# Kernel optimization log

Measured on AMD Instinct MI355X. Metric: run time of the kernel, lower is better.

## Reference

```python
import jax, jax.numpy as jnp
import numpy as np
import math

B, S, D = 16, 2048, 128

def setup_inputs() -> dict:
    key = jax.random.key(0)
    k1, k2, k3, k4 = jax.random.split(key, 4)
    query = jax.random.normal(k1, (B, S, D), dtype=jnp.float32)
    key_t = jax.random.normal(k2, (B, S, D), dtype=jnp.float32)
    value = jax.random.normal(k3, (B, S, D), dtype=jnp.float32)
    attn_mask = jax.random.randint(k4, (B, S, S), 0, 2).astype(bool)
    return {"query": query, "key": key_t, "value": value, "attn_mask": attn_mask}

def reference(query, key, value, attn_mask):
    # score = Q K^T / sqrt(d)  -> [B, Sq, Sk]
    scale = 1.0 / math.sqrt(query.shape[-1])
    score = jnp.einsum('bqd,bkd->bqk', query, key) * scale
    # faithful quirk: masked positions are replaced by the VALUE 1e-9 (not -inf)
    mask_score = jnp.where(attn_mask, jnp.float32(1e-9), score)
    # faithful quirk: softmax over dim=1 (the query axis), as in the torch source
    score_matrix = jax.nn.softmax(mask_score, axis=1)
    # output = softmax(scores) @ V  -> [B, Sq, D]
    output = jnp.einsum('bqk,bkd->bqd', score_matrix, value)
    return output
```

## Files before the change

### kernel.cpp

```cpp
#include <hip/hip_runtime.h>
#include <math.h>

#define NB 16
#define SS 2048
#define DQ 128
#define SCALE 0.08838834764831845f

typedef __bf16 bf16x8 __attribute__((ext_vector_type(8)));
typedef unsigned short ushort8_t __attribute__((ext_vector_type(8)));
typedef float floatx4 __attribute__((ext_vector_type(4)));

__device__ __forceinline__ unsigned short f2bf(float x) {
  unsigned int u = __float_as_uint(x);
  u += 0x7fffu + ((u >> 16) & 1u);
  return (unsigned short)(u >> 16);
}
union FragU { ushort8_t u; bf16x8 b; };
__device__ __forceinline__ bf16x8 ld_frag(const unsigned short* p) {
  FragU t; t.u = *(const ushort8_t*)p; return t.b;
}
__device__ __forceinline__ floatx4 mfma16(bf16x8 a, bf16x8 b, floatx4 c) {
  return __builtin_amdgcn_mfma_f32_16x16x32_bf16(a, b, c, 0, 0, 0);
}

__device__ __forceinline__ void bar_lds() {
  asm volatile("s_waitcnt lgkmcnt(0)\n\ts_barrier" ::: "memory");
}


__global__ void zero_accum(float* __restrict__ O) {
  float* p = O + (size_t)blockIdx.x * SS * DQ + 16 * DQ;
#pragma unroll
  for (int i = 0; i < 8; ++i) p[threadIdx.x + 256 * i] = 0.f;
}

__global__ __launch_bounds__(256, 4) void pass1_colsum(
    const float* __restrict__ Q, const float* __restrict__ K,
    const int* __restrict__ M, float* __restrict__ O)
{
  const int k0  = blockIdx.x * 64;
  const int b   = blockIdx.y;
  const int qc  = blockIdx.z;
  const int tid = threadIdx.x;
  const int w = tid >> 6, lane = tid & 63, l15 = lane & 15, quad = lane >> 4;

  __shared__ unsigned short Kbf[64][136];
  __shared__ unsigned short Qbf[64][136];
  __shared__ float red[4][64];

  const float* Qb = Q + (size_t)b * SS * DQ;
  const float* Kb = K + (size_t)b * SS * DQ;
  const int*   Mb = M + (size_t)b * SS * SS;

  const int srow = tid >> 5;
  const int sc4  = (tid & 31) * 4;

#pragma unroll
  for (int r = 0; r < 8; ++r) {
    int row = srow + r * 8;
    float4 v = *(const float4*)(Kb + (size_t)(k0 + row) * DQ + sc4);
    *(ushort4*)&Kbf[row][sc4] = make_ushort4(f2bf(v.x), f2bf(v.y), f2bf(v.z), f2bf(v.w));
  }

  const int qlane = 16 * w + l15;

  float4 qreg[8];
  int4 mv_nxt[4];
  {
    const int q0 = qc * 512;
#pragma unroll
    for (int r = 0; r < 8; ++r)
      qreg[r] = *(const float4*)(Qb + (size_t)(q0 + srow + r * 8) * DQ + sc4);
#pragma unroll
    for (int i = 0; i < 4; ++i)
      mv_nxt[i] = *(const int4*)(Mb + (size_t)(q0 + qlane) * SS + k0 + 16 * i + quad * 4);
  }

  float colacc[16];
#pragma unroll
  for (int t = 0; t < 16; ++t) colacc[t] = 0.f;

  for (int qi = 0; qi < 8; ++qi) {
    bar_lds();
    int4 mv[4] = {mv_nxt[0], mv_nxt[1], mv_nxt[2], mv_nxt[3]};
#pragma unroll
    for (int r = 0; r < 8; ++r) {
      float4 v = qreg[r];
      *(ushort4*)&Qbf[srow + r * 8][sc4] =
          make_ushort4(f2bf(v.x), f2bf(v.y), f2bf(v.z), f2bf(v.w));
    }
    bar_lds();
    if (qi < 7) {
      const int qn = qc * 512 + (qi + 1) * 64;
#pragma unroll
      for (int r = 0; r < 8; ++r)
        qreg[r] = *(const float4*)(Qb + (size_t)(qn + srow + r * 8) * DQ + sc4);
#pragma unroll
      for (int i = 0; i < 4; ++i)
        mv_nxt[i] = *(const int4*)(Mb + (size_t)(qn + qlane) * SS + k0 + 16 * i + quad * 4);
    }

    floatx4 acc[4];
#pragma unroll
    for (int i = 0; i < 4; ++i) acc[i] = (floatx4){0.f, 0.f, 0.f, 0.f};
#pragma unroll
    for (int d0 = 0; d0 < DQ; d0 += 32) {
      bf16x8 bq = ld_frag(&Qbf[qlane][d0 + quad * 8]);
#pragma unroll
      for (int i = 0; i < 4; ++i) {
        bf16x8 ak = ld_frag(&Kbf[16 * i + l15][d0 + quad * 8]);
        acc[i] = mfma16(ak, bq, acc[i]);
      }
    }
#pragma unroll
    for (int i = 0; i < 4; ++i) {
      int mm[4] = {mv[i].x, mv[i].y, mv[i].z, mv[i].w};
#pragma unroll
      for (int r = 0; r < 4; ++r) {
        float s = mm[r] ? 1e-9f : acc[i][r] * SCALE;
        colacc[i * 4 + r] += __expf(s);
      }
    }
  }

#pragma unroll
  for (int t = 0; t < 16; ++t) {
    colacc[t] += __shfl_xor(colacc[t], 1, 64);
    colacc[t] += __shfl_xor(colacc[t], 2, 64);
    colacc[t] += __shfl_xor(colacc[t], 4, 64);
    colacc[t] += __shfl_xor(colacc[t], 8, 64);
  }
  if (l15 == 0) {
#pragma unroll
    for (int i = 0; i < 4; ++i)
#pragma unroll
      for (int r = 0; r < 4; ++r)
        red[w][16 * i + quad * 4 + r] = colacc[i * 4 + r];
  }
  bar_lds();
  if (tid < 64) {
    float s = red[0][tid] + red[1][tid] + red[2][tid] + red[3][tid];
    atomicAdd(O + (size_t)b * SS * DQ + 16 * DQ + k0 + tid, s);
  }
}

__global__ void combine_linv(float* __restrict__ O) {
  const int b  = blockIdx.x;
  const int jb = blockIdx.y * 4;
  float* Ob = O + (size_t)b * SS * DQ;
#pragma unroll
  for (int it = 0; it < 8; ++it) {
    int k = threadIdx.x + 256 * it;
    float inv = 1.0f / Ob[16 * DQ + k];
#pragma unroll
    for (int j = 0; j < 4; ++j)
      Ob[(size_t)(64 * (jb + j)) * DQ + k] = inv;
  }
}

__global__ __launch_bounds__(256, 2) void pass2_out(
    const float* __restrict__ Q, const float* __restrict__ K,
    const float* __restrict__ V, const int* __restrict__ M,
    float* __restrict__ O)
{
  const int b = blockIdx.y, q0 = blockIdx.x * 64;
  const int tid = threadIdx.x;
  const int w = tid >> 6, lane = tid & 63, l15 = lane & 15, quad = lane >> 4;

  __shared__ unsigned short Kbf[64][136];
  __shared__ unsigned short Es[64][72];
  __shared__ unsigned short Wt[128][72];
  __shared__ float Li[SS];

  const float* Qb = Q + (size_t)b * SS * DQ;
  const float* Kb = K + (size_t)b * SS * DQ;
  const float* Vb = V + (size_t)b * SS * DQ;
  const int*   Mb = M + (size_t)b * SS * SS;

  const int srow = tid >> 5;
  const int sc4  = (tid & 31) * 4;

  {
    const float* src = O + ((size_t)b * SS + q0) * DQ;
#pragma unroll
    for (int r = 0; r < 2; ++r) {
      int idx = (tid + r * 256) * 4;
      *(float4*)&Li[idx] = *(const float4*)(src + idx);
    }
  }
  FragU qf[4];
  {
    const float* qrow = Qb + (size_t)(q0 + 16 * w + l15) * DQ;
#pragma unroll
    for (int i = 0; i < 4; ++i) {
      float4 a = *(const float4*)(qrow + 32 * i + quad * 8);
      float4 c = *(const float4*)(qrow + 32 * i + quad * 8 + 4);
      qf[i].u = (ushort8_t){f2bf(a.x), f2bf(a.y), f2bf(a.z), f2bf(a.w),
                            f2bf(c.x), f2bf(c.y), f2bf(c.z), f2bf(c.w)};
    }
  }

  floatx4 accO[8];
#pragma unroll
  for (int j = 0; j < 8; ++j) accO[j] = (floatx4){0.f, 0.f, 0.f, 0.f};

  const int* mrow = Mb + (size_t)(q0 + 16 * w + l15) * SS;

  float4 kreg[8], vreg[8];
  int4 mv_nxt[4];
  const int vk2 = (tid >> 5) * 2;
  {
#pragma unroll
    for (int r = 0; r < 8; ++r)
      kreg[r] = *(const float4*)(Kb + (size_t)(srow + r * 8) * DQ + sc4);
#pragma unroll
    for (int r = 0; r < 4; ++r) {
      int k2 = vk2 + r * 16;
      vreg[2 * r]     = *(const float4*)(Vb + (size_t)(k2)     * DQ + sc4);
      vreg[2 * r + 1] = *(const float4*)(Vb + (size_t)(k2 + 1) * DQ + sc4);
    }
#pragma unroll
    for (int j = 0; j < 4; ++j)
      mv_nxt[j] = *(const int4*)(mrow + 16 * j + quad * 4);
  }

  for (int k0 = 0; k0 < SS; k0 += 64) {
    bar_lds();
    int4 mv[4] = {mv_nxt[0], mv_nxt[1], mv_nxt[2], mv_nxt[3]};

#pragma unroll
    for (int r = 0; r < 8; ++r) {
      float4 v = kreg[r];
      *(ushort4*)&Kbf[srow + r * 8][sc4] =
          make_ushort4(f2bf(v.x), f2bf(v.y), f2bf(v.z), f2bf(v.w));
    }
#pragma unroll
    for (int r = 0; r < 4; ++r) {
      int k2 = vk2 + r * 16;
      float fa[4] = {vreg[2*r].x, vreg[2*r].y, vreg[2*r].z, vreg[2*r].w};
      float fb[4] = {vreg[2*r+1].x, vreg[2*r+1].y, vreg[2*r+1].z, vreg[2*r+1].w};
#pragma unroll
      for (int i = 0; i < 4; ++i) {
        int d  = sc4 + i;
        int kk = k2 ^ ((((unsigned)d >> 2) & 7) << 3);
        *(ushort2*)&Wt[d][kk] = make_ushort2(f2bf(fa[i]), f2bf(fb[i]));
      }
    }
    bar_lds();

    if (k0 + 64 < SS) {
      const int kn = k0 + 64;
#pragma unroll
      for (int r = 0; r < 8; ++r)
        kreg[r] = *(const float4*)(Kb + (size_t)(kn + srow + r * 8) * DQ + sc4);
#pragma unroll
      for (int r = 0; r < 4; ++r) {
        int k2 = vk2 + r * 16;
        vreg[2 * r]     = *(const float4*)(Vb + (size_t)(kn + k2)     * DQ + sc4);
        vreg[2 * r + 1] = *(const float4*)(Vb + (size_t)(kn + k2 + 1) * DQ + sc4);
      }
#pragma unroll
      for (int j = 0; j < 4; ++j)
        mv_nxt[j] = *(const int4*)(mrow + kn + 16 * j + quad * 4);
    }

    floatx4 acc[4];
#pragma unroll
    for (int j = 0; j < 4; ++j) acc[j] = (floatx4){0.f, 0.f, 0.f, 0.f};
#pragma unroll
    for (int i = 0; i < 4; ++i) {
      bf16x8 bq = qf[i].b;
#pragma unroll
      for (int j = 0; j < 4; ++j) {
        bf16x8 ak = ld_frag(&Kbf[16 * j + l15][32 * i + quad * 8]);
        acc[j] = mfma16(ak, bq, acc[j]);
      }
    }
#pragma unroll
    for (int j = 0; j < 4; ++j) {
      float4 liv = *(const float4*)&Li[k0 + 16 * j + quad * 4];
      float lv[4] = {liv.x, liv.y, liv.z, liv.w};
      int mm[4] = {mv[j].x, mv[j].y, mv[j].z, mv[j].w};
      unsigned short es[4];
#pragma unroll
      for (int r = 0; r < 4; ++r) {
        float s = mm[r] ? 1e-9f : acc[j][r] * SCALE;
        es[r] = f2bf(__expf(s) * lv[r]);
      }
      *(ushort4*)&Es[16 * w + l15][16 * j + quad * 4] =
          make_ushort4(es[0], es[1], es[2], es[3]);
    }
#pragma unroll
    for (int c = 0; c < 2; ++c) {
      bf16x8 be = ld_frag(&Es[16 * w + l15][32 * c + quad * 8]);
#pragma unroll
      for (int j = 0; j < 8; ++j) {
        int d  = 16 * j + l15;
        int kk = (32 * c + quad * 8) ^ ((((unsigned)d >> 2) & 7) << 3);
        bf16x8 aw = ld_frag(&Wt[d][kk]);
        accO[j] = mfma16(aw, be, accO[j]);
      }
    }
  }

#pragma unroll
  for (int j = 0; j < 8; ++j) {
    float* op = O + ((size_t)b * SS + q0 + 16 * w + l15) * DQ + 16 * j + quad * 4;
    *(float4*)op = make_float4(accO[j][0], accO[j][1], accO[j][2], accO[j][3]);
  }
}

extern "C" void kernel_launch(void* const* d_in, const int* in_sizes, int n_in,
                              void* d_out, int out_size, void* d_ws, size_t ws_size,
                              hipStream_t stream) {
  const float* Q = (const float*)d_in[0];
  const float* K = (const float*)d_in[1];
  const float* V = (const float*)d_in[2];
  const int*   M = (const int*)d_in[3];
  float* O = (float*)d_out;
  (void)d_ws; (void)ws_size;

  zero_accum<<<dim3(NB), 256, 0, stream>>>(O);
  pass1_colsum<<<dim3(32, NB, 4), 256, 0, stream>>>(Q, K, M, O);
  combine_linv<<<dim3(NB, 8), 256, 0, stream>>>(O);
  pass2_out<<<dim3(32, NB), 256, 0, stream>>>(Q, K, V, M, O);
}
```

Baseline: 518.1 us.

## Materialize bf16 exp scores in workspace so pass 2 skips QK recompute

Pass 1 now also writes exp(score) as bf16 into a B*S*S workspace buffer when the workspace is large enough. A new pass2_pv kernel reads those values instead of recomputing QK^T and re-reading the int32 mask, then scales V by the inverse column sums and runs the PV MFMA. This removes the second QK^T matmul and the second read of the mask, at the cost of writing and reading a 128 MB bf16 intermediate and depending on the harness supplying that much workspace. If the workspace is missing or too small, the old path runs.

Result: no change. 513.5 us (-0.9%).

```diff
diff --git a/kernel.cpp b/kernel.cpp
--- a/kernel.cpp
+++ b/kernel.cpp
@@ -34,9 +34,11 @@
   for (int i = 0; i < 8; ++i) p[threadIdx.x + 256 * i] = 0.f;
 }
 
+template<int WRITE_E>
 __global__ __launch_bounds__(256, 4) void pass1_colsum(
     const float* __restrict__ Q, const float* __restrict__ K,
-    const int* __restrict__ M, float* __restrict__ O)
+    const int* __restrict__ M, float* __restrict__ O,
+    unsigned short* __restrict__ E)
 {
   const int k0  = blockIdx.x * 64;
   const int b   = blockIdx.y;
@@ -51,6 +53,7 @@
   const float* Qb = Q + (size_t)b * SS * DQ;
   const float* Kb = K + (size_t)b * SS * DQ;
   const int*   Mb = M + (size_t)b * SS * SS;
+  unsigned short* Eb = WRITE_E ? (E + (size_t)b * SS * SS) : nullptr;
 
   const int srow = tid >> 5;
   const int sc4  = (tid & 31) * 4;
@@ -112,13 +115,20 @@
         acc[i] = mfma16(ak, bq, acc[i]);
       }
     }
+    const int qrow = qc * 512 + qi * 64 + qlane;
 #pragma unroll
     for (int i = 0; i < 4; ++i) {
       int mm[4] = {mv[i].x, mv[i].y, mv[i].z, mv[i].w};
+      float ev[4];
 #pragma unroll
       for (int r = 0; r < 4; ++r) {
         float s = mm[r] ? 1e-9f : acc[i][r] * SCALE;
-        colacc[i * 4 + r] += __expf(s);
+        ev[r] = __expf(s);
+        colacc[i * 4 + r] += ev[r];
+      }
+      if (WRITE_E) {
+        *(ushort4*)(Eb + (size_t)qrow * SS + k0 + 16 * i + quad * 4) =
+            make_ushort4(f2bf(ev[0]), f2bf(ev[1]), f2bf(ev[2]), f2bf(ev[3]));
       }
     }
   }
@@ -155,6 +165,105 @@
 #pragma unroll
     for (int j = 0; j < 4; ++j)
       Ob[(size_t)(64 * (jb + j)) * DQ + k] = inv;
+  }
+}
+
+__global__ __launch_bounds__(256, 2) void pass2_pv(
+    const float* __restrict__ V, const unsigned short* __restrict__ E,
+    float* __restrict__ O)
+{
+  const int b = blockIdx.y, q0 = blockIdx.x * 64;
+  const int tid = threadIdx.x;
+  const int w = tid >> 6, lane = tid & 63, l15 = lane & 15, quad = lane >> 4;
+
+  __shared__ unsigned short Wt[128][72];
+  __shared__ float Li[SS];
+
+  const float* Vb = V + (size_t)b * SS * DQ;
+  const unsigned short* Erow =
+      E + (size_t)b * SS * SS + (size_t)(q0 + 16 * w + l15) * SS;
+
+  const int sc4 = (tid & 31) * 4;
+  const int vk2 = (tid >> 5) * 2;
+
+  {
+    const float* src = O + ((size_t)b * SS + q0) * DQ;
+#pragma unroll
+    for (int r = 0; r < 2; ++r) {
+      int idx = (tid + r * 256) * 4;
+      *(float4*)&Li[idx] = *(const float4*)(src + idx);
+    }
+  }
+
+  floatx4 accO[8];
+#pragma unroll
+  for (int j = 0; j < 8; ++j) accO[j] = (floatx4){0.f, 0.f, 0.f, 0.f};
+
+  float4 vreg[8];
+  FragU ef_nxt[2];
+  {
+#pragma unroll
+    for (int r = 0; r < 4; ++r) {
+      int k2 = vk2 + r * 16;
+      vreg[2 * r]     = *(const float4*)(Vb + (size_t)(k2)     * DQ + sc4);
+      vreg[2 * r + 1] = *(const float4*)(Vb + (size_t)(k2 + 1) * DQ + sc4);
+    }
+#pragma unroll
+    for (int c = 0; c < 2; ++c)
+      ef_nxt[c].u = *(const ushort8_t*)(Erow + 32 * c + quad * 8);
+  }
+
+  for (int k0 = 0; k0 < SS; k0 += 64) {
+    bar_lds();
+    FragU ef[2] = {ef_nxt[0], ef_nxt[1]};
+
+#pragma unroll
+    for (int r = 0; r < 4; ++r) {
+      int k2 = vk2 + r * 16;
+      float la = Li[k0 + k2], lb = Li[k0 + k2 + 1];
+      float fa[4] = {vreg[2*r].x * la, vreg[2*r].y * la,
+                     vreg[2*r].z * la, vreg[2*r].w * la};
+      float fb[4] = {vreg[2*r+1].x * lb, vreg[2*r+1].y * lb,
+                     vreg[2*r+1].z * lb, vreg[2*r+1].w * lb};
+#pragma unroll
+      for (int i = 0; i < 4; ++i) {
+        int d  = sc4 + i;
+        int kk = k2 ^ ((((unsigned)d >> 2) & 7) << 3);
+        *(ushort2*)&Wt[d][kk] = make_ushort2(f2bf(fa[i]), f2bf(fb[i]));
+      }
+    }
+    bar_lds();
+
+    if (k0 + 64 < SS) {
+      const int kn = k0 + 64;
+#pragma unroll
+      for (int r = 0; r < 4; ++r) {
+        int k2 = vk2 + r * 16;
+        vreg[2 * r]     = *(const float4*)(Vb + (size_t)(kn + k2)     * DQ + sc4);
+        vreg[2 * r + 1] = *(const float4*)(Vb + (size_t)(kn + k2 + 1) * DQ + sc4);
+      }
+#pragma unroll
+      for (int c = 0; c < 2; ++c)
+        ef_nxt[c].u = *(const ushort8_t*)(Erow + kn + 32 * c + quad * 8);
+    }
+
+#pragma unroll
+    for (int c = 0; c < 2; ++c) {
+      bf16x8 be = ef[c].b;
+#pragma unroll
+      for (int j = 0; j < 8; ++j) {
+        int d  = 16 * j + l15;
+        int kk = (32 * c + quad * 8) ^ ((((unsigned)d >> 2) & 7) << 3);
+        bf16x8 aw = ld_frag(&Wt[d][kk]);
+        accO[j] = mfma16(aw, be, accO[j]);
+      }
+    }
+  }
+
+#pragma unroll
+  for (int j = 0; j < 8; ++j) {
+    float* op = O + ((size_t)b * SS + q0 + 16 * w + l15) * DQ + 16 * j + quad * 4;
+    *(float4*)op = make_float4(accO[j][0], accO[j][1], accO[j][2], accO[j][3]);
   }
 }
 
@@ -318,10 +427,18 @@
   const float* V = (const float*)d_in[2];
   const int*   M = (const int*)d_in[3];
   float* O = (float*)d_out;
-  (void)d_ws; (void)ws_size;
+
+  const size_t eneed = (size_t)NB * SS * SS * sizeof(unsigned short);
 
   zero_accum<<<dim3(NB), 256, 0, stream>>>(O);
-  pass1_colsum<<<dim3(32, NB, 4), 256, 0, stream>>>(Q, K, M, O);
-  combine_linv<<<dim3(NB, 8), 256, 0, stream>>>(O);
-  pass2_out<<<dim3(32, NB), 256, 0, stream>>>(Q, K, V, M, O);
-}
+  if (d_ws != nullptr && ws_size >= eneed) {
+    unsigned short* E = (unsigned short*)d_ws;
+    pass1_colsum<1><<<dim3(32, NB, 4), 256, 0, stream>>>(Q, K, M, O, E);
+    combine_linv<<<dim3(NB, 8), 256, 0, stream>>>(O);
+    pass2_pv<<<dim3(32, NB), 256, 0, stream>>>(V, E, O);
+  } else {
+    pass1_colsum<0><<<dim3(32, NB, 4), 256, 0, stream>>>(Q, K, M, O, nullptr);
+    combine_linv<<<dim3(NB, 8), 256, 0, stream>>>(O);
+    pass2_out<<<dim3(32, NB), 256, 0, stream>>>(Q, K, V, M, O);
+  }
+}
```
